# Performance work log

Hardware: AMD Instinct MI355X
Metric: run time of the kernel (lower is better)

The kernel has to match this reference:

```python
import jax, jax.numpy as jnp
import numpy as np


def _ktk(kz):
    t = np.arange(kz, dtype=np.float64)
    A = np.ones((kz * kz, 3))
    A[:, 0] = np.repeat(t, kz)   # temp.repeat(kz)
    A[:, 1] = np.tile(t, kz)     # temp.repeat(kz).reshape(kz,kz).T.reshape(-1)
    k = A @ np.linalg.inv(A.T @ A) @ A.T - np.eye(kz * kz)
    return jnp.asarray(k.T @ k, dtype=jnp.float32)


def _patches(g, kz):
    # g: (b, H, W) -> (b, kz*kz, h, w) with patch index q = a*kz + c for offset (a, c),
    # matching torch conv2d weight flattening (valid padding, stride 1).
    return jax.lax.conv_general_dilated_patches(
        g[:, None, :, :], filter_shape=(kz, kz), window_strides=(1, 1),
        padding='VALID')


def _affine_loss(flow, kz, KTK):
    # flow: (b, 2, H, W), H == W (original code uses arange(w) for both axes)
    W = flow.shape[-1]
    coord = jnp.arange(W, dtype=flow.dtype)
    gx = flow[:, 0] + coord[None, None, :]   # x = column index grid
    gy = flow[:, 1] + coord[None, :, None]   # y = row index grid

    def chan_loss(g):
        P = _patches(g, kz)  # (b, kz^2, h, w)
        # conv2d(grid, KTK rows) -> R_q = sum_r KTK[q,r] P_r ;
        # BlockExtractor(f=kz//2) + LocalAttnReshape + mul + avg_pool(kz)*kz^2 + mean
        # == mean over (b,h,w) of p^T KTK p
        return jnp.mean(jnp.einsum('bqhw,qr,brhw->bhw', P, KTK, P))

    return chan_loss(gx) + chan_loss(gy)


def setup_inputs() -> dict:
    key = jax.random.key(0)
    k0, k1 = jax.random.split(key)
    flow0 = jax.random.normal(k0, (32, 2, 128, 128), dtype=jnp.float32)
    flow1 = jax.random.normal(k1, (32, 2, 256, 256), dtype=jnp.float32)
    return {"flow0": flow0, "flow1": flow1}


def reference(flow0, flow1):
    # kz_dic = {"2": 5, "3": 3}; layers = sorted(keys, reverse=True) = ["3", "2"]
    loss = _affine_loss(flow0, 3, _ktk(3))
    loss = loss + _affine_loss(flow1, 5, _ktk(5))
    return loss
```

## Files before the change

### kernel.cpp

```cpp
#include <hip/hip_runtime.h>


template<int KZ>
__global__ void patch_loss_kernel(const float* __restrict__ flow,
                                  int W, int Wout, int npix,
                                  float scale, float* __restrict__ partial) {
    const float m = (KZ - 1) * 0.5f;
    float Ssum = 0.f;
#pragma unroll
    for (int t = 0; t < KZ; ++t) Ssum += (t - m) * (t - m);
    const float invS = 1.0f / (Ssum * KZ);
    const float invk2 = 1.0f / (KZ * KZ);
    const int HW = W * W;

    float acc = 0.f;
    for (int idx = blockIdx.x * blockDim.x + threadIdx.x; idx < npix;
         idx += gridDim.x * blockDim.x) {
        int x  = idx % Wout;
        int t1 = idx / Wout;
        int y  = t1 % Wout;
        int bc = t1 / Wout;
        const float* base = flow + (size_t)bc * HW + (size_t)y * W + x;

        float sum = 0.f, sumsq = 0.f, sa = 0.f, sc = 0.f;
#pragma unroll
        for (int a = 0; a < KZ; ++a) {
#pragma unroll
            for (int c = 0; c < KZ; ++c) {
                float p = base[a * W + c];
                sum   += p;
                sumsq += p * p;
                sa    += (a - m) * p;
                sc    += (c - m) * p;
            }
        }
        acc += sumsq - sum * sum * invk2 - (sa * sa + sc * sc) * invS;
    }

    for (int off = 32; off > 0; off >>= 1) acc += __shfl_down(acc, off);
    __shared__ float red[4];
    int lane = threadIdx.x & 63;
    int wid  = threadIdx.x >> 6;
    if (lane == 0) red[wid] = acc;
    __syncthreads();
    if (threadIdx.x == 0)
        partial[blockIdx.x] = (red[0] + red[1] + red[2] + red[3]) * scale;
}

__global__ void final_reduce_kernel(const float* __restrict__ partial, int n,
                                    float* __restrict__ out) {
    float acc = 0.f;
    for (int i = threadIdx.x; i < n; i += blockDim.x) acc += partial[i];
    for (int off = 32; off > 0; off >>= 1) acc += __shfl_down(acc, off);
    __shared__ float red[4];
    int lane = threadIdx.x & 63;
    int wid  = threadIdx.x >> 6;
    if (lane == 0) red[wid] = acc;
    __syncthreads();
    if (threadIdx.x == 0) out[0] = red[0] + red[1] + red[2] + red[3];
}

extern "C" void kernel_launch(void* const* d_in, const int* in_sizes, int n_in,
                              void* d_out, int out_size, void* d_ws, size_t ws_size,
                              hipStream_t stream) {
    const float* flow0 = (const float*)d_in[0];
    const float* flow1 = (const float*)d_in[1];
    float* out = (float*)d_out;
    float* partial = (float*)d_ws;

    constexpr int NB0 = 1024;
    constexpr int NB1 = 2048;

    {
        int W = 128, Wout = 126;
        int npix = 32 * 2 * Wout * Wout;
        float scale = 1.0f / (32.0f * Wout * Wout);
        patch_loss_kernel<3><<<NB0, 256, 0, stream>>>(flow0, W, Wout, npix, scale,
                                                      partial);
    }
    {
        int W = 256, Wout = 252;
        int npix = 32 * 2 * Wout * Wout;
        float scale = 1.0f / (32.0f * Wout * Wout);
        patch_loss_kernel<5><<<NB1, 256, 0, stream>>>(flow1, W, Wout, npix, scale,
                                                      partial + NB0);
    }
    final_reduce_kernel<<<1, 256, 0, stream>>>(partial, NB0 + NB1, out);
}
```

Baseline: 92.30 us.

## Fuse both scales into one kernel with multi-pixel vectorized patch sums and atomics

Merges the two per-scale launches and the final reduction into a single kernel. Blocks are split by index between the 3x3 and 5x5 workloads, and each block adds its partial sum atomically into an output that is zeroed with a memset. Each thread now computes 2 (3x3) or 4 (5x5) adjacent output pixels from vectorized float2/float4 row loads, reusing the overlapping window data through prefix sums. This cuts launch overhead, redundant global loads and index arithmetic, at the cost of hardcoded shapes and a nondeterministic float atomic summation order.

```diff
diff --git a/kernel.cpp b/kernel.cpp
--- a/kernel.cpp
+++ b/kernel.cpp
@@ -1,40 +1,89 @@
 #include <hip/hip_runtime.h>
 
 
-template<int KZ>
-__global__ void patch_loss_kernel(const float* __restrict__ flow,
-                                  int W, int Wout, int npix,
-                                  float scale, float* __restrict__ partial) {
-    const float m = (KZ - 1) * 0.5f;
-    float Ssum = 0.f;
+#define NB0 256
+#define NB1 1792
+
+__global__ __launch_bounds__(256) void fused_affine_loss_kernel(
+    const float* __restrict__ f0, const float* __restrict__ f1,
+    float* __restrict__ out) {
+    float acc = 0.f;
+
+    if (blockIdx.x < NB0) {
+        constexpr int W = 128, ROWS = 126, SPR = 63;
+        constexpr int NST = 64 * ROWS * SPR;
+        const float invk2 = 1.f / 9.f;
+        const float invS  = 1.f / 6.f;
+        for (int idx = blockIdx.x * 256 + threadIdx.x; idx < NST;
+             idx += NB0 * 256) {
+            int si = idx % SPR;
+            int t  = idx / SPR;
+            int y  = t % ROWS;
+            int bc = t / ROWS;
+            const float* base = f0 + (size_t)bc * (W * W) + y * W + si * 2;
+
+            float sum0 = 0.f, sq0 = 0.f, sa0 = 0.f, sc0 = 0.f;
+            float sum1 = 0.f, sq1 = 0.f, sa1 = 0.f, sc1 = 0.f;
 #pragma unroll
-    for (int t = 0; t < KZ; ++t) Ssum += (t - m) * (t - m);
-    const float invS = 1.0f / (Ssum * KZ);
-    const float invk2 = 1.0f / (KZ * KZ);
-    const int HW = W * W;
+            for (int a = 0; a < 3; ++a) {
+                const float* r = base + a * W;
+                float2 u = *(const float2*)r;
+                float2 v = *(const float2*)(r + 2);
+                float p0 = u.x, p1 = u.y, p2 = v.x, p3 = v.y;
+                float rs0 = p0 + p1 + p2, rs1 = p1 + p2 + p3;
+                float rq0 = p0 * p0 + p1 * p1 + p2 * p2;
+                float rq1 = p1 * p1 + p2 * p2 + p3 * p3;
+                float aw = (float)(a - 1);
+                sum0 += rs0; sq0 += rq0; sa0 += aw * rs0; sc0 += p2 - p0;
+                sum1 += rs1; sq1 += rq1; sa1 += aw * rs1; sc1 += p3 - p1;
+            }
+            acc += sq0 - sum0 * sum0 * invk2 - (sa0 * sa0 + sc0 * sc0) * invS;
+            acc += sq1 - sum1 * sum1 * invk2 - (sa1 * sa1 + sc1 * sc1) * invS;
+        }
+        acc *= 1.0f / (32.0f * 126.0f * 126.0f);
+    } else {
+        constexpr int W = 256, ROWS = 252, SPR = 63;
+        constexpr int NST = 64 * ROWS * SPR;
+        const float invk2 = 1.f / 25.f;
+        const float invS  = 1.f / 50.f;
+        for (int idx = (blockIdx.x - NB0) * 256 + threadIdx.x; idx < NST;
+             idx += NB1 * 256) {
+            int si = idx % SPR;
+            int t  = idx / SPR;
+            int y  = t % ROWS;
+            int bc = t / ROWS;
+            const float* base = f1 + (size_t)bc * (W * W) + y * W + si * 4;
 
-    float acc = 0.f;
-    for (int idx = blockIdx.x * blockDim.x + threadIdx.x; idx < npix;
-         idx += gridDim.x * blockDim.x) {
-        int x  = idx % Wout;
-        int t1 = idx / Wout;
-        int y  = t1 % Wout;
-        int bc = t1 / Wout;
-        const float* base = flow + (size_t)bc * HW + (size_t)y * W + x;
-
-        float sum = 0.f, sumsq = 0.f, sa = 0.f, sc = 0.f;
+            float sum[4] = {0, 0, 0, 0}, sq[4] = {0, 0, 0, 0};
+            float sa[4] = {0, 0, 0, 0}, sc[4] = {0, 0, 0, 0};
 #pragma unroll
-        for (int a = 0; a < KZ; ++a) {
+            for (int a = 0; a < 5; ++a) {
+                const float* r = base + a * W;
+                float4 u = *(const float4*)r;
+                float4 v = *(const float4*)(r + 4);
+                float p[8] = {u.x, u.y, u.z, u.w, v.x, v.y, v.z, v.w};
+                float pre[8], prq[8];
+                pre[0] = p[0]; prq[0] = p[0] * p[0];
 #pragma unroll
-            for (int c = 0; c < KZ; ++c) {
-                float p = base[a * W + c];
-                sum   += p;
-                sumsq += p * p;
-                sa    += (a - m) * p;
-                sc    += (c - m) * p;
+                for (int i = 1; i < 8; ++i) {
+                    pre[i] = pre[i - 1] + p[i];
+                    prq[i] = prq[i - 1] + p[i] * p[i];
+                }
+                float aw = (float)(a - 2);
+#pragma unroll
+                for (int j = 0; j < 4; ++j) {
+                    float rs = (j == 0) ? pre[4] : pre[j + 4] - pre[j - 1];
+                    float rq = (j == 0) ? prq[4] : prq[j + 4] - prq[j - 1];
+                    float rc = (p[j + 3] - p[j + 1]) + 2.f * (p[j + 4] - p[j]);
+                    sum[j] += rs; sq[j] += rq; sa[j] += aw * rs; sc[j] += rc;
+                }
             }
+#pragma unroll
+            for (int j = 0; j < 4; ++j)
+                acc += sq[j] - sum[j] * sum[j] * invk2
+                     - (sa[j] * sa[j] + sc[j] * sc[j]) * invS;
         }
-        acc += sumsq - sum * sum * invk2 - (sa * sa + sc * sc) * invS;
+        acc *= 1.0f / (32.0f * 252.0f * 252.0f);
     }
 
     for (int off = 32; off > 0; off >>= 1) acc += __shfl_down(acc, off);
@@ -44,20 +93,7 @@
     if (lane == 0) red[wid] = acc;
     __syncthreads();
     if (threadIdx.x == 0)
-        partial[blockIdx.x] = (red[0] + red[1] + red[2] + red[3]) * scale;
-}
-
-__global__ void final_reduce_kernel(const float* __restrict__ partial, int n,
-                                    float* __restrict__ out) {
-    float acc = 0.f;
-    for (int i = threadIdx.x; i < n; i += blockDim.x) acc += partial[i];
-    for (int off = 32; off > 0; off >>= 1) acc += __shfl_down(acc, off);
-    __shared__ float red[4];
-    int lane = threadIdx.x & 63;
-    int wid  = threadIdx.x >> 6;
-    if (lane == 0) red[wid] = acc;
-    __syncthreads();
-    if (threadIdx.x == 0) out[0] = red[0] + red[1] + red[2] + red[3];
+        atomicAdd(out, red[0] + red[1] + red[2] + red[3]);
 }
 
 extern "C" void kernel_launch(void* const* d_in, const int* in_sizes, int n_in,
@@ -66,24 +102,7 @@
     const float* flow0 = (const float*)d_in[0];
     const float* flow1 = (const float*)d_in[1];
     float* out = (float*)d_out;
-    float* partial = (float*)d_ws;
 
-    constexpr int NB0 = 1024;
-    constexpr int NB1 = 2048;
-
-    {
-        int W = 128, Wout = 126;
-        int npix = 32 * 2 * Wout * Wout;
-        float scale = 1.0f / (32.0f * Wout * Wout);
-        patch_loss_kernel<3><<<NB0, 256, 0, stream>>>(flow0, W, Wout, npix, scale,
-                                                      partial);
-    }
-    {
-        int W = 256, Wout = 252;
-        int npix = 32 * 2 * Wout * Wout;
-        float scale = 1.0f / (32.0f * Wout * Wout);
-        patch_loss_kernel<5><<<NB1, 256, 0, stream>>>(flow1, W, Wout, npix, scale,
-                                                      partial + NB0);
-    }
-    final_reduce_kernel<<<1, 256, 0, stream>>>(partial, NB0 + NB1, out);
+    hipMemsetAsync(out, 0, sizeof(float), stream);
+    fused_affine_loss_kernel<<<NB0 + NB1, 256, 0, stream>>>(flow0, flow1, out);
 }
```

After: 94.50 us. 2.4% more time.
